# Performance work log

Measured on AMD Instinct MI355X. Metric: run time of the kernel, lower is better.

Reference implementation:

```python
import jax, jax.numpy as jnp
import numpy as np

N = 50000
E = 800000
IN_C = 128
HID = 32
HEADS = 4
OUT_C = 128
NEG_SLOPE = 0.2


def setup_inputs() -> dict:
    key = jax.random.key(0)
    ks = jax.random.split(key, 12)
    x = jax.random.normal(ks[0], (N, IN_C), dtype=jnp.float32)
    edge_index = jax.random.randint(ks[1], (2, E), 0, N, dtype=jnp.int32)
    s1 = 1.0 / np.sqrt(IN_C)
    s2 = 1.0 / np.sqrt(HEADS * HID)
    return {
        "x": x,
        "edge_index": edge_index,
        # conv1: in_channels -> hidden*heads, concat=True
        "W1l": jax.random.normal(ks[2], (IN_C, HEADS * HID), dtype=jnp.float32) * s1,
        "W1r": jax.random.normal(ks[3], (IN_C, HEADS * HID), dtype=jnp.float32) * s1,
        "att1": jax.random.normal(ks[4], (HEADS, HID), dtype=jnp.float32) * (1.0 / np.sqrt(HID)),
        "b1": jnp.zeros((HEADS * HID,), dtype=jnp.float32),
        # conv2: hidden*heads -> out_channels, heads=1, concat=False
        "W2l": jax.random.normal(ks[5], (HEADS * HID, OUT_C), dtype=jnp.float32) * s2,
        "W2r": jax.random.normal(ks[6], (HEADS * HID, OUT_C), dtype=jnp.float32) * s2,
        "att2": jax.random.normal(ks[7], (1, OUT_C), dtype=jnp.float32) * (1.0 / np.sqrt(OUT_C)),
        "b2": jnp.zeros((OUT_C,), dtype=jnp.float32),
    }


def gatv2_conv(x, src, dst, Wl, Wr, att, bias, heads, out_per_head, concat):
    n = x.shape[0]
    xl = (x @ Wl).reshape(n, heads, out_per_head)   # source transform [N,H,C]
    xr = (x @ Wr).reshape(n, heads, out_per_head)   # target transform [N,H,C]
    m = xl[src] + xr[dst]                           # [E,H,C]
    e = jnp.sum(jax.nn.leaky_relu(m, NEG_SLOPE) * att, axis=-1)  # [E,H]
    # segment softmax over incoming edges of each destination node
    mx = jax.ops.segment_max(e, dst, num_segments=n)             # [N,H]
    ex = jnp.exp(e - mx[dst])                                    # [E,H]
    denom = jax.ops.segment_sum(ex, dst, num_segments=n)         # [N,H]
    alpha = ex / jnp.where(denom[dst] == 0, 1.0, denom[dst])     # [E,H]
    out = jax.ops.segment_sum(alpha[:, :, None] * xl[src], dst, num_segments=n)  # [N,H,C]
    if concat:
        out = out.reshape(n, heads * out_per_head)
    else:
        out = out.mean(axis=1)
    return out + bias


def reference(x, edge_index, W1l, W1r, att1, b1, W2l, W2r, att2, b2):
    src, dst = edge_index[0], edge_index[1]
    h = gatv2_conv(x, src, dst, W1l, W1r, att1, b1, HEADS, HID, concat=True)
    h = jax.nn.elu(h)
    out = gatv2_conv(h, src, dst, W2l, W2r, att2, b2, 1, OUT_C, concat=False)
    return out
```

## Files before the change

### kernel.cpp

```cpp
#include <hip/hip_runtime.h>
#include <math.h>

#define IN_C 128
#define NEG_SLOPE 0.2f
#define LOG2E 1.44269504f

typedef unsigned int uint_t;
typedef unsigned short ushort_t;
typedef _Float16 half8_t __attribute__((ext_vector_type(8)));
typedef _Float16 half2_t __attribute__((ext_vector_type(2)));
typedef float floatx4 __attribute__((ext_vector_type(4)));

__device__ __forceinline__ float fdot2f(half2_t a, half2_t b, float c) {
#if __has_builtin(__builtin_amdgcn_fdot2)
    return __builtin_amdgcn_fdot2(a, b, c, false);
#else
    return fmaf((float)a[1], (float)b[1], fmaf((float)a[0], (float)b[0], c));
#endif
}
#define H2(v, i) ((half2_t){(v)[2 * (i)], (v)[2 * (i) + 1]})

__device__ __forceinline__ float fexp2(float x) {
#if __has_builtin(__builtin_amdgcn_exp2f)
    return __builtin_amdgcn_exp2f(x);
#else
    return exp2f(x);
#endif
}

template <int CTRL>
__device__ __forceinline__ float dpp_addf(float x) {
    int y = __builtin_amdgcn_update_dpp(0, __float_as_int(x), CTRL, 0xF, 0xF, true);
    return x + __int_as_float(y);
}

#define XPAD 136
template <bool IN_HALF>
__global__ __launch_bounds__(256) void transform_mfma(
        const void* __restrict__ xin,
        const float* __restrict__ Wl,
        const float* __restrict__ Wr,
        _Float16* __restrict__ outl,
        _Float16* __restrict__ outr, int n) {
    __shared__ _Float16 xs[16 * XPAD + 8];
    const int tid  = threadIdx.x;
    const int wv   = tid >> 6;
    const int l    = tid & 63;
    const int lm   = l & 15;
    const int quad = l >> 4;
    const int kb   = quad * 8;

    const float* Wsel = (wv < 2) ? Wl : Wr;
    _Float16*    osel = (wv < 2) ? outl : outr;
    const int nbase = (wv & 1) * 64;
    half8_t bw[4][4];
#pragma unroll
    for (int t = 0; t < 4; ++t) {
        const int ncol = nbase + t * 16 + lm;
#pragma unroll
        for (int K = 0; K < 4; ++K) {
            const int k0 = K * 32 + kb;
            half8_t h;
#pragma unroll
            for (int j = 0; j < 8; ++j)
                h[j] = (_Float16)Wsel[(size_t)(k0 + j) * IN_C + ncol];
            bw[t][K] = h;
        }
    }

    const int nStrips = (n + 15) >> 4;
    for (int s = blockIdx.x; s < nStrips; s += gridDim.x) {
        const int row0 = s * 16;
        __syncthreads();
        {
            const int srow = tid >> 4;
            const int scol = (tid & 15) * 8;
            const int grow = row0 + srow;
            half8_t h;
#pragma unroll
            for (int j = 0; j < 8; ++j) h[j] = (_Float16)0.f;
            if (grow < n) {
                if constexpr (IN_HALF) {
                    h = *(const half8_t*)&((const _Float16*)xin)[(size_t)grow * IN_C + scol];
                } else {
                    const float4 v0 = *(const float4*)&((const float*)xin)[(size_t)grow * IN_C + scol];
                    const float4 v1 = *(const float4*)&((const float*)xin)[(size_t)grow * IN_C + scol + 4];
                    h[0] = (_Float16)v0.x; h[1] = (_Float16)v0.y;
                    h[2] = (_Float16)v0.z; h[3] = (_Float16)v0.w;
                    h[4] = (_Float16)v1.x; h[5] = (_Float16)v1.y;
                    h[6] = (_Float16)v1.z; h[7] = (_Float16)v1.w;
                }
            }
            *(half8_t*)&xs[srow * XPAD + scol] = h;
        }
        __syncthreads();
        half8_t af[4];
#pragma unroll
        for (int K = 0; K < 4; ++K)
            af[K] = *(half8_t*)&xs[lm * XPAD + K * 32 + kb];
        floatx4 acc[4];
#pragma unroll
        for (int t = 0; t < 4; ++t) acc[t] = (floatx4){0.f, 0.f, 0.f, 0.f};
#pragma unroll
        for (int t = 0; t < 4; ++t)
#pragma unroll
            for (int K = 0; K < 4; ++K)
                acc[t] = __builtin_amdgcn_mfma_f32_16x16x32_f16(af[K], bw[t][K], acc[t], 0, 0, 0);
#pragma unroll
        for (int t = 0; t < 4; ++t) {
            const int col = nbase + t * 16 + lm;
#pragma unroll
            for (int r = 0; r < 4; ++r) {
                const int row = row0 + quad * 4 + r;
                if (row < n) osel[(size_t)row * IN_C + col] = (_Float16)acc[t][r];
            }
        }
    }
}

__global__ void hist_kernel(const int* __restrict__ dst, int* __restrict__ cnt,
                            ushort_t* __restrict__ rank, int E) {
    int e = blockIdx.x * blockDim.x + threadIdx.x;
    if (e < E) {
        int r = atomicAdd(&cnt[dst[e]], 1);
        rank[e] = (ushort_t)r;
    }
}

__global__ void scan_block_sums(const int* __restrict__ cnt, int* __restrict__ part, int n) {
    __shared__ int sdata[256];
    int t = threadIdx.x;
    int i = blockIdx.x * 256 + t;
    sdata[t] = (i < n) ? ((cnt[i] + 3) & ~3) : 0;
    __syncthreads();
    for (int o = 128; o >= 1; o >>= 1) {
        if (t < o) sdata[t] += sdata[t + o];
        __syncthreads();
    }
    if (t == 0) part[blockIdx.x] = sdata[0];
}

__global__ void scan_part_excl(int* __restrict__ part, int nb) {
    __shared__ int buf[1024];
    int t = threadIdx.x;
    int v = (t < nb) ? part[t] : 0;
    buf[t] = v;
    __syncthreads();
    for (int o = 1; o < 1024; o <<= 1) {
        int a = (t >= o) ? buf[t - o] : 0;
        __syncthreads();
        buf[t] += a;
        __syncthreads();
    }
    if (t < nb) part[t] = buf[t] - v;
}

__global__ void scan_final(const int* __restrict__ cnt, const int* __restrict__ part,
                           int* __restrict__ rowptr, ushort_t* __restrict__ gsrc, int n) {
    __shared__ int buf[256];
    int t = threadIdx.x;
    int i = blockIdx.x * 256 + t;
    int deg = (i < n) ? cnt[i] : 0;
    int v = (deg + 3) & ~3;
    buf[t] = v;
    __syncthreads();
    for (int o = 1; o < 256; o <<= 1) {
        int a = (t >= o) ? buf[t - o] : 0;
        __syncthreads();
        buf[t] += a;
        __syncthreads();
    }
    int excl = part[blockIdx.x] + buf[t] - v;
    if (i < n) {
        rowptr[i] = excl;
        for (int p = excl + deg; p < excl + v; ++p) gsrc[p] = 0;
    }
    if (i == n - 1) rowptr[n] = excl + v;
}

__global__ void scatter_csr(const int* __restrict__ src,
                            const int* __restrict__ dst,
                            const int* __restrict__ rowptr,
                            const ushort_t* __restrict__ rank,
                            ushort_t* __restrict__ gsrc, int E) {
    int e = blockIdx.x * blockDim.x + threadIdx.x;
    if (e >= E) return;
    int pos = rowptr[dst[e]] + (int)rank[e];
    gsrc[pos] = (ushort_t)src[e];
}

template <int LAYER>
__global__ __launch_bounds__(256) void node_fused(
        const _Float16* __restrict__ xlb,
        const _Float16* __restrict__ xr,
        const float* __restrict__ att,
        const int* __restrict__ rowptr,
        const int* __restrict__ cnt,
        const ushort_t* __restrict__ gsrc,
        const float* __restrict__ bias,
        void* __restrict__ outp, int N) {
    const int l = threadIdx.x & 63;
    const int q = l & 15;
    const int d = blockIdx.x * 16 + (threadIdx.x >> 4);
    if (d >= N) return;
    const int beg = rowptr[d];
    const int deg = cnt[d];
    const int nt  = (deg + 3) >> 2;
    const int cb  = q * 8;

    const half8_t xrv = *(const half8_t*)&xr[(size_t)d * IN_C + cb];
    const float4 A0 = *(const float4*)&att[cb];
    const float4 A1 = *(const float4*)&att[cb + 4];
    const float afv[8] = {A0.x, A0.y, A0.z, A0.w, A1.x, A1.y, A1.z, A1.w};
    half8_t a6, a4;
#pragma unroll
    for (int j = 0; j < 8; ++j) {
        a6[j] = (_Float16)(0.6f * LOG2E * afv[j]);
        a4[j] = (_Float16)(0.4f * LOG2E * afv[j]);
    }

    float m = -1e30f, ls = 0.f;
    float acc[8] = {0.f, 0.f, 0.f, 0.f, 0.f, 0.f, 0.f, 0.f};

    const uint2* gp = (const uint2*)(gsrc + beg);
    half8_t xc[4], xn[4];
    uint2 g2;
    if (nt > 0) {
        uint2 g0 = gp[0];
        uint2 g1 = gp[(1 < nt) ? 1 : 0];
        g2 = gp[(2 < nt) ? 2 : nt - 1];
        uint_t i0 = g0.x & 0xffffu, i1 = g0.x >> 16;
        uint_t i2 = g0.y & 0xffffu, i3 = g0.y >> 16;
        xc[0] = *(const half8_t*)(xlb + (i0 << 7) + cb);
        xc[1] = *(const half8_t*)(xlb + (i1 << 7) + cb);
        xc[2] = *(const half8_t*)(xlb + (i2 << 7) + cb);
        xc[3] = *(const half8_t*)(xlb + (i3 << 7) + cb);
        i0 = g1.x & 0xffffu; i1 = g1.x >> 16;
        i2 = g1.y & 0xffffu; i3 = g1.y >> 16;
        xn[0] = *(const half8_t*)(xlb + (i0 << 7) + cb);
        xn[1] = *(const half8_t*)(xlb + (i1 << 7) + cb);
        xn[2] = *(const half8_t*)(xlb + (i2 << 7) + cb);
        xn[3] = *(const half8_t*)(xlb + (i3 << 7) + cb);
    }

    for (int t = 0; t < nt; ++t) {
        const int t3 = (t + 3 < nt) ? t + 3 : nt - 1;
        uint2 g3 = gp[t3];
        half8_t x2[4];
        {
            uint_t i0 = g2.x & 0xffffu, i1 = g2.x >> 16;
            uint_t i2 = g2.y & 0xffffu, i3 = g2.y >> 16;
            x2[0] = *(const half8_t*)(xlb + (i0 << 7) + cb);
            x2[1] = *(const half8_t*)(xlb + (i1 << 7) + cb);
            x2[2] = *(const half8_t*)(xlb + (i2 << 7) + cb);
            x2[3] = *(const half8_t*)(xlb + (i3 << 7) + cb);
        }
        float f[4];
#pragma unroll
        for (int u = 0; u < 4; ++u) {
            half8_t tv = xc[u] + xrv;
            uint4 tu = __builtin_bit_cast(uint4, tv);
            tu.x &= 0x7fff7fffu; tu.y &= 0x7fff7fffu;
            tu.z &= 0x7fff7fffu; tu.w &= 0x7fff7fffu;
            half8_t av = __builtin_bit_cast(half8_t, tu);
            float p = 0.f;
#pragma unroll
            for (int j = 0; j < 4; ++j) p = fdot2f(H2(tv, j), H2(a6, j), p);
#pragma unroll
            for (int j = 0; j < 4; ++j) p = fdot2f(H2(av, j), H2(a4, j), p);
            p = dpp_addf<0xB1>(p);
            p = dpp_addf<0x4E>(p);
            if (LAYER == 2) {
                p = dpp_addf<0x141>(p);
                p = dpp_addf<0x140>(p);
            }
            f[u] = (4 * t + u < deg) ? p : -1e30f;
        }
        float bm = fmaxf(fmaxf(f[0], f[1]), fmaxf(f[2], f[3]));
        if (!__all(bm <= m + 5.7708f)) {
            float nm = fmaxf(m, bm);
            float fc = fexp2(m - nm);
            ls *= fc;
#pragma unroll
            for (int j = 0; j < 8; ++j) acc[j] *= fc;
            m = nm;
        }
#pragma unroll
        for (int u = 0; u < 4; ++u) {
            float wgt = fexp2(f[u] - m);
            ls += wgt;
#pragma unroll
            for (int j = 0; j < 8; ++j)
                acc[j] = fmaf((float)xc[u][j], wgt, acc[j]);
        }
#pragma unroll
        for (int u = 0; u < 4; ++u) { xc[u] = xn[u]; xn[u] = x2[u]; }
        g2 = g3;
    }

    const float inv = (ls > 0.f) ? 1.f / ls : 0.f;
    const float4 b0 = *(const float4*)&bias[cb];
    const float4 b1 = *(const float4*)&bias[cb + 4];
    const float bf[8] = {b0.x, b0.y, b0.z, b0.w, b1.x, b1.y, b1.z, b1.w};
    if (LAYER == 1) {
        half8_t h;
#pragma unroll
        for (int j = 0; j < 8; ++j) {
            float o = acc[j] * inv + bf[j];
            o = (o > 0.f) ? o : fexp2(o * LOG2E) - 1.f;
            h[j] = (_Float16)o;
        }
        *(half8_t*)&((_Float16*)outp)[(size_t)d * IN_C + cb] = h;
    } else {
        float4 o1, o2;
        o1.x = acc[0] * inv + bf[0]; o1.y = acc[1] * inv + bf[1];
        o1.z = acc[2] * inv + bf[2]; o1.w = acc[3] * inv + bf[3];
        o2.x = acc[4] * inv + bf[4]; o2.y = acc[5] * inv + bf[5];
        o2.z = acc[6] * inv + bf[6]; o2.w = acc[7] * inv + bf[7];
        *(float4*)&((float*)outp)[(size_t)d * IN_C + cb]     = o1;
        *(float4*)&((float*)outp)[(size_t)d * IN_C + cb + 4] = o2;
    }
}

extern "C" void kernel_launch(void* const* d_in, const int* in_sizes, int n_in,
                              void* d_out, int out_size, void* d_ws, size_t ws_size,
                              hipStream_t stream) {
    const float* x    = (const float*)d_in[0];
    const int*   ei   = (const int*)d_in[1];
    const float* W1l  = (const float*)d_in[2];
    const float* W1r  = (const float*)d_in[3];
    const float* att1 = (const float*)d_in[4];
    const float* b1   = (const float*)d_in[5];
    const float* W2l  = (const float*)d_in[6];
    const float* W2r  = (const float*)d_in[7];
    const float* att2 = (const float*)d_in[8];
    const float* b2   = (const float*)d_in[9];

    const int N = in_sizes[0] / IN_C;
    const int E = in_sizes[1] / 2;
    const int* src = ei;
    const int* dst = ei + E;

    float* ws = (float*)d_ws;
    size_t o = 0;
    _Float16* xlh = (_Float16*)(ws + o); o += (size_t)N * IN_C / 2;
    _Float16* xrh = (_Float16*)(ws + o); o += (size_t)N * IN_C / 2;
    _Float16* hb  = (_Float16*)(ws + o); o += (size_t)N * IN_C / 2;
    int* iws    = (int*)(ws + o);
    int* rowptr = iws;
    int* cnt    = rowptr + (N + 1);
    int* part   = cnt + N;
    ushort_t* rank = (ushort_t*)(part + 1024);
    ushort_t* gsrc = rank + ((size_t)E + 64);
    (void)ws_size;

    hipMemsetAsync(cnt, 0, (size_t)N * 4, stream);

    const int B = 256;
    const int nb = (N + 255) / 256;
    hist_kernel<<<(E + B - 1) / B, B, 0, stream>>>(dst, cnt, rank, E);
    scan_block_sums<<<nb, 256, 0, stream>>>(cnt, part, N);
    scan_part_excl<<<1, 1024, 0, stream>>>(part, nb);
    scan_final<<<nb, 256, 0, stream>>>(cnt, part, rowptr, gsrc, N);
    scatter_csr<<<(E + B - 1) / B, B, 0, stream>>>(src, dst, rowptr, rank, gsrc, E);

    transform_mfma<false><<<512, 256, 0, stream>>>(x, W1l, W1r, xlh, xrh, N);
    node_fused<1><<<(N + 15) / 16, 256, 0, stream>>>(xlh, xrh, att1, rowptr, cnt, gsrc, b1, hb, N);

    transform_mfma<true><<<512, 256, 0, stream>>>(hb, W2l, W2r, xlh, xrh, N);
    node_fused<2><<<(N + 15) / 16, 256, 0, stream>>>(xlh, xrh, att2, rowptr, cnt, gsrc, b2, d_out, N);
}
```

Measured before the change: 247.2 us.

## Fuse CSR construction into a single cooperative kernel with grid syncs

Replaces the memset plus five separate CSR-building kernels (histogram, block sums, partial scan, final scan, scatter) with one cooperative kernel of 1024 blocks that uses grid-wide syncs between phases. This removes several kernel launches and their inter-kernel gaps. In exchange, each phase runs with a fixed grid and grid-stride loops, and the cooperative grid syncs add their own cost. The partial-sum scan now runs in a single 256-thread block, which assumes at most 256 chunks (N ≤ 65536).

```diff
diff --git a/kernel.cpp b/kernel.cpp
--- a/kernel.cpp
+++ b/kernel.cpp
@@ -1,9 +1,13 @@
 #include <hip/hip_runtime.h>
+#include <hip/hip_cooperative_groups.h>
 #include <math.h>
+
+namespace cg = cooperative_groups;
 
 #define IN_C 128
 #define NEG_SLOPE 0.2f
 #define LOG2E 1.44269504f
+#define CSRB 1024
 
 typedef unsigned int uint_t;
 typedef unsigned short ushort_t;
@@ -118,75 +122,75 @@
     }
 }
 
-__global__ void hist_kernel(const int* __restrict__ dst, int* __restrict__ cnt,
-                            ushort_t* __restrict__ rank, int E) {
-    int e = blockIdx.x * blockDim.x + threadIdx.x;
-    if (e < E) {
+__global__ __launch_bounds__(256) void csr_build(
+        const int* __restrict__ src, const int* __restrict__ dst,
+        int* __restrict__ cnt, ushort_t* __restrict__ rank,
+        int* __restrict__ rowptr, int* __restrict__ part,
+        ushort_t* __restrict__ gsrc, int N, int E) {
+    cg::grid_group grid = cg::this_grid();
+    __shared__ int sdata[256];
+    const int tid = threadIdx.x;
+    const int gsz = gridDim.x * 256;
+    const int gid = blockIdx.x * 256 + tid;
+    const int nchunks = (N + 255) >> 8;
+
+    for (int i = gid; i < N; i += gsz) cnt[i] = 0;
+    grid.sync();
+    for (int e = gid; e < E; e += gsz) {
         int r = atomicAdd(&cnt[dst[e]], 1);
         rank[e] = (ushort_t)r;
     }
-}
-
-__global__ void scan_block_sums(const int* __restrict__ cnt, int* __restrict__ part, int n) {
-    __shared__ int sdata[256];
-    int t = threadIdx.x;
-    int i = blockIdx.x * 256 + t;
-    sdata[t] = (i < n) ? ((cnt[i] + 3) & ~3) : 0;
-    __syncthreads();
-    for (int o = 128; o >= 1; o >>= 1) {
-        if (t < o) sdata[t] += sdata[t + o];
-        __syncthreads();
-    }
-    if (t == 0) part[blockIdx.x] = sdata[0];
-}
-
-__global__ void scan_part_excl(int* __restrict__ part, int nb) {
-    __shared__ int buf[1024];
-    int t = threadIdx.x;
-    int v = (t < nb) ? part[t] : 0;
-    buf[t] = v;
-    __syncthreads();
-    for (int o = 1; o < 1024; o <<= 1) {
-        int a = (t >= o) ? buf[t - o] : 0;
-        __syncthreads();
-        buf[t] += a;
-        __syncthreads();
-    }
-    if (t < nb) part[t] = buf[t] - v;
-}
-
-__global__ void scan_final(const int* __restrict__ cnt, const int* __restrict__ part,
-                           int* __restrict__ rowptr, ushort_t* __restrict__ gsrc, int n) {
-    __shared__ int buf[256];
-    int t = threadIdx.x;
-    int i = blockIdx.x * 256 + t;
-    int deg = (i < n) ? cnt[i] : 0;
-    int v = (deg + 3) & ~3;
-    buf[t] = v;
-    __syncthreads();
-    for (int o = 1; o < 256; o <<= 1) {
-        int a = (t >= o) ? buf[t - o] : 0;
-        __syncthreads();
-        buf[t] += a;
-        __syncthreads();
-    }
-    int excl = part[blockIdx.x] + buf[t] - v;
-    if (i < n) {
-        rowptr[i] = excl;
-        for (int p = excl + deg; p < excl + v; ++p) gsrc[p] = 0;
-    }
-    if (i == n - 1) rowptr[n] = excl + v;
-}
-
-__global__ void scatter_csr(const int* __restrict__ src,
-                            const int* __restrict__ dst,
-                            const int* __restrict__ rowptr,
-                            const ushort_t* __restrict__ rank,
-                            ushort_t* __restrict__ gsrc, int E) {
-    int e = blockIdx.x * blockDim.x + threadIdx.x;
-    if (e >= E) return;
-    int pos = rowptr[dst[e]] + (int)rank[e];
-    gsrc[pos] = (ushort_t)src[e];
+    grid.sync();
+    for (int c = blockIdx.x; c < nchunks; c += gridDim.x) {
+        int i = c * 256 + tid;
+        sdata[tid] = (i < N) ? ((cnt[i] + 3) & ~3) : 0;
+        __syncthreads();
+        for (int o = 128; o >= 1; o >>= 1) {
+            if (tid < o) sdata[tid] += sdata[tid + o];
+            __syncthreads();
+        }
+        if (tid == 0) part[c] = sdata[0];
+        __syncthreads();
+    }
+    grid.sync();
+    if (blockIdx.x == 0) {
+        int v = (tid < nchunks) ? part[tid] : 0;
+        sdata[tid] = v;
+        __syncthreads();
+        for (int o = 1; o < 256; o <<= 1) {
+            int a = (tid >= o) ? sdata[tid - o] : 0;
+            __syncthreads();
+            sdata[tid] += a;
+            __syncthreads();
+        }
+        if (tid < nchunks) part[tid] = sdata[tid] - v;
+    }
+    grid.sync();
+    for (int c = blockIdx.x; c < nchunks; c += gridDim.x) {
+        int i = c * 256 + tid;
+        int deg = (i < N) ? cnt[i] : 0;
+        int v = (deg + 3) & ~3;
+        sdata[tid] = v;
+        __syncthreads();
+        for (int o = 1; o < 256; o <<= 1) {
+            int a = (tid >= o) ? sdata[tid - o] : 0;
+            __syncthreads();
+            sdata[tid] += a;
+            __syncthreads();
+        }
+        int excl = part[c] + sdata[tid] - v;
+        if (i < N) {
+            rowptr[i] = excl;
+            for (int p = excl + deg; p < excl + v; ++p) gsrc[p] = 0;
+        }
+        if (i == N - 1) rowptr[N] = excl + v;
+        __syncthreads();
+    }
+    grid.sync();
+    for (int e = gid; e < E; e += gsz) {
+        int pos = rowptr[dst[e]] + (int)rank[e];
+        gsrc[pos] = (ushort_t)src[e];
+    }
 }
 
 template <int LAYER>
@@ -354,15 +358,13 @@
     ushort_t* gsrc = rank + ((size_t)E + 64);
     (void)ws_size;
 
-    hipMemsetAsync(cnt, 0, (size_t)N * 4, stream);
-
-    const int B = 256;
-    const int nb = (N + 255) / 256;
-    hist_kernel<<<(E + B - 1) / B, B, 0, stream>>>(dst, cnt, rank, E);
-    scan_block_sums<<<nb, 256, 0, stream>>>(cnt, part, N);
-    scan_part_excl<<<1, 1024, 0, stream>>>(part, nb);
-    scan_final<<<nb, 256, 0, stream>>>(cnt, part, rowptr, gsrc, N);
-    scatter_csr<<<(E + B - 1) / B, B, 0, stream>>>(src, dst, rowptr, rank, gsrc, E);
+    {
+        void* args[] = {(void*)&src, (void*)&dst, (void*)&cnt, (void*)&rank,
+                        (void*)&rowptr, (void*)&part, (void*)&gsrc,
+                        (void*)&N, (void*)&E};
+        hipLaunchCooperativeKernel((const void*)csr_build, dim3(CSRB), dim3(256),
+                                   args, 0, stream);
+    }
 
     transform_mfma<false><<<512, 256, 0, stream>>>(x, W1l, W1r, xlh, xrh, N);
     node_fused<1><<<(N + 15) / 16, 256, 0, stream>>>(xlh, xrh, att1, rowptr, cnt, gsrc, b1, hb, N);
```

Measured after the change: 727.3 us. +194.2%, slower.
